# Kernel optimization log

Hardware: AMD Instinct MI355X
Metric: run time of the kernel (lower is better)

## Reference

```python
import jax, jax.numpy as jnp
import numpy as np

D_TEXT, D_AUDIO, D_HID = 1024, 768, 1024
EPS = 1e-5


def layer_norm(x, gamma, beta):
    mu = jnp.mean(x, axis=-1, keepdims=True)
    var = jnp.mean(jnp.square(x - mu), axis=-1, keepdims=True)
    return (x - mu) * jax.lax.rsqrt(var + EPS) * gamma + beta


def setup_inputs() -> dict:
    key = jax.random.key(0)
    ks = jax.random.split(key, 8)
    B, L, S = 16, 1024, 2048
    # xavier_uniform bound = sqrt(6/(fan_in+fan_out))
    def xavier(k, shape):
        bound = np.sqrt(6.0 / (shape[0] + shape[1]))
        return jax.random.uniform(k, shape, jnp.float32, -bound, bound)
    return {
        "H_l": jax.random.normal(ks[0], (B, L, D_TEXT), jnp.float32),
        "H_a": jax.random.normal(ks[1], (B, S, D_AUDIO), jnp.float32),
        "W_text": xavier(ks[2], (D_TEXT, D_HID)),
        "b_text": jnp.zeros((D_HID,), jnp.float32),
        "W_audio": xavier(ks[3], (D_AUDIO, D_HID)),
        "b_audio": jnp.zeros((D_HID,), jnp.float32),
        "W_out": xavier(ks[4], (D_HID, D_HID)),
        "b_out": jnp.zeros((D_HID,), jnp.float32),
        "g1": jnp.ones((D_HID,), jnp.float32),
        "beta1": jnp.zeros((D_HID,), jnp.float32),
        "g2": jnp.ones((D_HID,), jnp.float32),
        "beta2": jnp.zeros((D_HID,), jnp.float32),
        "g_out": jnp.ones((D_HID,), jnp.float32),
        "beta_out": jnp.zeros((D_HID,), jnp.float32),
    }


def reference(H_l, H_a, W_text, b_text, W_audio, b_audio, W_out, b_out,
              g1, beta1, g2, beta2, g_out, beta_out):
    # projections
    text_p = jnp.einsum('bld,dh->blh', H_l, W_text) + b_text    # [B,L,H]
    audio_p = jnp.einsum('bsd,dh->bsh', H_a, W_audio) + b_audio  # [B,S,H]
    Q = layer_norm(text_p, g1, beta1)
    K = layer_norm(audio_p, g2, beta2)
    V = audio_p
    scale = 1.0 / np.sqrt(D_HID).astype(np.float32)
    scores = jnp.einsum('blh,bsh->bls', Q, K) * scale            # [B,L,S]
    alpha = jax.nn.softmax(scores, axis=-1)
    # dropout is identity in eval mode
    H_hyper = jnp.einsum('bls,bsh->blh', alpha, V)               # [B,L,H]
    H_hyper = jnp.einsum('blh,hk->blk', H_hyper, W_out) + b_out
    return layer_norm(H_hyper + H_l, g_out, beta_out)
```

## Files before the change

kernel.cpp:

```cpp
#include <hip/hip_runtime.h>
#include <cstdio>

typedef unsigned short u16;
typedef __bf16 bf16x8 __attribute__((ext_vector_type(8)));
typedef float f32x4 __attribute__((ext_vector_type(4)));
typedef unsigned short us4 __attribute__((ext_vector_type(4)));
typedef unsigned short us8 __attribute__((ext_vector_type(8)));

__device__ __forceinline__ u16 f2bf(float f) {
    union { float f; unsigned u; } x; x.f = f;
    unsigned u = x.u + 0x7fffu + ((x.u >> 16) & 1u);
    return (u16)(u >> 16);
}
__device__ __forceinline__ float bf2f(u16 u) {
    union { unsigned u; float f; } x; x.u = ((unsigned)u) << 16;
    return x.f;
}


#define LDFRAG(base, row, koff) \
  (*(const bf16x8*)((const char*)(base) + (size_t)(row) * 128 + \
                    ((koff) ^ (((row) & 7) << 4))))

#define LOAD_A(QM) do { \
  _Pragma("unroll") for (int j = 0; j < 4; ++j) \
    _Pragma("unroll") for (int ks = 0; ks < 2; ++ks) \
      af[j][ks] = LDFRAG(pA, wr * 128 + (QM) * 64 + j * 16 + fr, ks * 64 + kg * 16); \
} while (0)

#define LOAD_B(QN) do { \
  _Pragma("unroll") for (int i = 0; i < 2; ++i) \
    _Pragma("unroll") for (int ks = 0; ks < 2; ++ks) \
      bfr[QN][i][ks] = LDFRAG(pB, wc * 64 + (QN) * 32 + i * 16 + fr, ks * 64 + kg * 16); \
} while (0)

#define MFMA_Q(QM, QN) do { \
  _Pragma("unroll") for (int j = 0; j < 4; ++j) \
    _Pragma("unroll") for (int i = 0; i < 2; ++i) \
      _Pragma("unroll") for (int ks = 0; ks < 2; ++ks) \
        acc[(QM) * 4 + j][(QN) * 2 + i] = __builtin_amdgcn_mfma_f32_16x16x32_bf16( \
            af[j][ks], bfr[QN][i][ks], acc[(QM) * 4 + j][(QN) * 2 + i], 0, 0, 0); \
} while (0)

#define PHASE_SYNC() do { \
  __builtin_amdgcn_s_barrier(); \
  asm volatile("s_waitcnt lgkmcnt(0)" ::: "memory"); \
  __builtin_amdgcn_sched_barrier(0); \
} while (0)

template<int TAG, bool HAS_BIAS, bool HAS_RESID, bool OUT_BF16>
__global__ __launch_bounds__(512, 2)
void gemm_nt(const u16* __restrict__ A, const u16* __restrict__ Bm,
             void* __restrict__ Cm, const float* __restrict__ bias,
             const float* __restrict__ resid,
             int K, int lda, int ldb, int ldc,
             long sA, long sB, long sC, float scale)
{
    __shared__ __align__(16) u16 lA[2 * 256 * 64];
    __shared__ __align__(16) u16 lB[2 * 256 * 64];

    const int tid = threadIdx.x;
    const long bz = blockIdx.z;
    A  += bz * sA;
    Bm += bz * sB;
    const long cbase = bz * sC;

    int bx, by;
    if (gridDim.z == 1) {
        const int gx = gridDim.x;
        const int flat = blockIdx.y * gx + blockIdx.x;
        const int q = (gx * gridDim.y) >> 3;
        const int wg = (flat & 7) * q + (flat >> 3);
        const int per = gx << 3;
        const int band = wg / per, rem = wg % per;
        bx = rem % gx;
        by = band * 8 + rem / gx;
    } else {
        bx = blockIdx.x; by = blockIdx.y;
    }
    const int m0 = by * 256;
    const int n0 = bx * 256;

    const int lane = tid & 63;
    const int w  = tid >> 6;
    const int wr = w >> 2, wc = w & 3;
    const int fr = lane & 15;
    const int kg = lane >> 4;

    auto stage_half = [&](int d_, int kt, int op, int h) {
        const u16* src = op ? Bm : A;
        const int  ld  = op ? ldb : lda;
        const int  bs  = op ? n0 : m0;
        u16* lds = (op ? lB : lA) + d_ * 16384 + h * 8192;
#pragma unroll
        for (int i2 = 0; i2 < 2; ++i2) {
            const int c  = i2 * 512 + tid;
            const int r  = c >> 3;
            const int kb = ((c & 7) * 16) ^ ((r & 7) << 4);
            const u16* g = src + (size_t)(bs + h * 128 + r) * ld + kt * 64 + (kb >> 1);
            __builtin_amdgcn_global_load_lds(
                (const __attribute__((address_space(1))) void*)g,
                (__attribute__((address_space(3))) void*)(lds + (size_t)c * 8), 16, 0, 0);
        }
    };
    auto stage_tile = [&](int d_, int kt) {
        stage_half(d_, kt, 0, 0); stage_half(d_, kt, 0, 1);
        stage_half(d_, kt, 1, 0); stage_half(d_, kt, 1, 1);
    };

    f32x4 acc[8][4] = {};
    bf16x8 af[4][2];
    bf16x8 bfr[2][2][2];

    const int nt = K >> 6;
    stage_tile(0, 0);

    for (int T = 0; T < nt; ++T) {
        const int d = T & 1;
        const u16* pA = lA + d * 16384;
        const u16* pB = lB + d * 16384;

        if (T + 1 < nt) {
            stage_tile(d ^ 1, T + 1);
            asm volatile("s_waitcnt vmcnt(8)" ::: "memory");
        } else {
            asm volatile("s_waitcnt vmcnt(0)" ::: "memory");
        }
        __builtin_amdgcn_s_barrier();

        LOAD_A(0); LOAD_B(0);
        PHASE_SYNC();
        __builtin_amdgcn_s_setprio(1); MFMA_Q(0, 0); __builtin_amdgcn_s_setprio(0);
        __builtin_amdgcn_s_barrier();

        LOAD_B(1);
        PHASE_SYNC();
        __builtin_amdgcn_s_setprio(1); MFMA_Q(0, 1); __builtin_amdgcn_s_setprio(0);
        __builtin_amdgcn_s_barrier();

        LOAD_A(1);
        PHASE_SYNC();
        __builtin_amdgcn_s_setprio(1); MFMA_Q(1, 0); __builtin_amdgcn_s_setprio(0);
        __builtin_amdgcn_s_barrier();

        __builtin_amdgcn_s_setprio(1); MFMA_Q(1, 1); __builtin_amdgcn_s_setprio(0);
    }

    const int orow = m0 + wr * 128 + kg * 4;
    const int ocol = n0 + wc * 64 + fr;
#pragma unroll
    for (int mf = 0; mf < 8; ++mf) {
#pragma unroll
        for (int r = 0; r < 4; ++r) {
            const int m = orow + mf * 16 + r;
#pragma unroll
            for (int nf = 0; nf < 4; ++nf) {
                const int n = ocol + nf * 16;
                float v = acc[mf][nf][r] * scale;
                if (HAS_BIAS)  v += bias[n];
                if (HAS_RESID) v += resid[cbase + (long)m * ldc + n];
                if (OUT_BF16)  ((u16*)Cm)[cbase + (long)m * ldc + n] = f2bf(v);
                else           ((float*)Cm)[cbase + (long)m * ldc + n] = v;
            }
        }
    }
}

template<bool IN_BF16, bool OUT_BF16>
__global__ __launch_bounds__(256)
void ln1024(const void* in, const float* __restrict__ g,
            const float* __restrict__ beta, void* out)
{
    const long row = blockIdx.x;
    const int tid = threadIdx.x;
    float x0, x1, x2, x3;
    if (IN_BF16) {
        const us4 v = ((const us4*)in)[row * 256 + tid];
        x0 = bf2f(v[0]); x1 = bf2f(v[1]); x2 = bf2f(v[2]); x3 = bf2f(v[3]);
    } else {
        const float4 v = ((const float4*)in)[row * 256 + tid];
        x0 = v.x; x1 = v.y; x2 = v.z; x3 = v.w;
    }
    float s  = x0 + x1 + x2 + x3;
    float s2 = x0 * x0 + x1 * x1 + x2 * x2 + x3 * x3;
#pragma unroll
    for (int off = 32; off > 0; off >>= 1) {
        s  += __shfl_xor(s, off);
        s2 += __shfl_xor(s2, off);
    }
    __shared__ float rs[4], rq[4];
    if ((tid & 63) == 0) { rs[tid >> 6] = s; rq[tid >> 6] = s2; }
    __syncthreads();
    const float S  = rs[0] + rs[1] + rs[2] + rs[3];
    const float S2 = rq[0] + rq[1] + rq[2] + rq[3];
    const float mu = S * (1.0f / 1024.0f);
    const float var = S2 * (1.0f / 1024.0f) - mu * mu;
    const float rstd = rsqrtf(var + 1e-5f);
    const float4 gg = ((const float4*)g)[tid];
    const float4 bb = ((const float4*)beta)[tid];
    const float y0 = (x0 - mu) * rstd * gg.x + bb.x;
    const float y1 = (x1 - mu) * rstd * gg.y + bb.y;
    const float y2 = (x2 - mu) * rstd * gg.z + bb.z;
    const float y3 = (x3 - mu) * rstd * gg.w + bb.w;
    if (OUT_BF16) {
        us4 o; o[0] = f2bf(y0); o[1] = f2bf(y1); o[2] = f2bf(y2); o[3] = f2bf(y3);
        ((us4*)out)[row * 256 + tid] = o;
    } else {
        float4 o; o.x = y0; o.y = y1; o.z = y2; o.w = y3;
        ((float4*)out)[row * 256 + tid] = o;
    }
}

__global__ __launch_bounds__(256)
void softmax2048_bf16(u16* io)
{
    const long row = blockIdx.x;
    const int tid = threadIdx.x;
    const us8 v = ((const us8*)io)[row * 256 + tid];
    float x[8];
#pragma unroll
    for (int i = 0; i < 8; ++i) x[i] = bf2f(v[i]);
    float m = x[0];
#pragma unroll
    for (int i = 1; i < 8; ++i) m = fmaxf(m, x[i]);
#pragma unroll
    for (int off = 32; off > 0; off >>= 1) m = fmaxf(m, __shfl_xor(m, off));
    __shared__ float rm[4], rsum[4];
    if ((tid & 63) == 0) rm[tid >> 6] = m;
    __syncthreads();
    m = fmaxf(fmaxf(rm[0], rm[1]), fmaxf(rm[2], rm[3]));
    float e[8];
    float s = 0.f;
#pragma unroll
    for (int i = 0; i < 8; ++i) { e[i] = __expf(x[i] - m); s += e[i]; }
#pragma unroll
    for (int off = 32; off > 0; off >>= 1) s += __shfl_xor(s, off);
    if ((tid & 63) == 0) rsum[tid >> 6] = s;
    __syncthreads();
    s = rsum[0] + rsum[1] + rsum[2] + rsum[3];
    const float inv = 1.0f / s;
    us8 o;
#pragma unroll
    for (int i = 0; i < 8; ++i) o[i] = f2bf(e[i] * inv);
    ((us8*)io)[row * 256 + tid] = o;
}

__global__ __launch_bounds__(256)
void cast_f32_bf16(const float* __restrict__ in, u16* __restrict__ out, long n8)
{
    const long i = (long)blockIdx.x * 256 + threadIdx.x;
    if (i >= n8) return;
    const float4 a = ((const float4*)in)[i * 2];
    const float4 b = ((const float4*)in)[i * 2 + 1];
    us8 o;
    o[0] = f2bf(a.x); o[1] = f2bf(a.y); o[2] = f2bf(a.z); o[3] = f2bf(a.w);
    o[4] = f2bf(b.x); o[5] = f2bf(b.y); o[6] = f2bf(b.z); o[7] = f2bf(b.w);
    ((us8*)out)[i] = o;
}

__global__ __launch_bounds__(256)
void tcast_f32_bf16(const float* __restrict__ in, u16* __restrict__ out,
                    int R, int C)
{
    __shared__ float t[32][33];
    const int tx = threadIdx.x, ty = threadIdx.y;
    const int c0 = blockIdx.x * 32, r0 = blockIdx.y * 32;
#pragma unroll
    for (int i = 0; i < 4; ++i)
        t[ty + i * 8][tx] = in[(long)(r0 + ty + i * 8) * C + c0 + tx];
    __syncthreads();
#pragma unroll
    for (int i = 0; i < 4; ++i)
        out[(long)(c0 + ty + i * 8) * R + r0 + tx] = f2bf(t[tx][ty + i * 8]);
}

__global__ __launch_bounds__(256)
void t_bf16_batched(const u16* __restrict__ in, u16* __restrict__ out,
                    int R, int C)
{
    __shared__ u16 t[32][34];
    const int tx = threadIdx.x, ty = threadIdx.y;
    const int c0 = blockIdx.x * 32, r0 = blockIdx.y * 32;
    const long base = (long)blockIdx.z * R * C;
#pragma unroll
    for (int i = 0; i < 4; ++i)
        t[ty + i * 8][tx] = in[base + (long)(r0 + ty + i * 8) * C + c0 + tx];
    __syncthreads();
#pragma unroll
    for (int i = 0; i < 4; ++i)
        out[base + (long)(c0 + ty + i * 8) * R + r0 + tx] = t[tx][ty + i * 8];
}

extern "C" void kernel_launch(void* const* d_in, const int* in_sizes, int n_in,
                              void* d_out, int out_size, void* d_ws, size_t ws_size,
                              hipStream_t stream)
{
    const float* H_l      = (const float*)d_in[0];
    const float* H_a      = (const float*)d_in[1];
    const float* W_text   = (const float*)d_in[2];
    const float* b_text   = (const float*)d_in[3];
    const float* W_audio  = (const float*)d_in[4];
    const float* b_audio  = (const float*)d_in[5];
    const float* W_out    = (const float*)d_in[6];
    const float* b_out    = (const float*)d_in[7];
    const float* g1       = (const float*)d_in[8];
    const float* beta1    = (const float*)d_in[9];
    const float* g2       = (const float*)d_in[10];
    const float* beta2    = (const float*)d_in[11];
    const float* g_out    = (const float*)d_in[12];
    const float* beta_out = (const float*)d_in[13];
    (void)in_sizes; (void)n_in; (void)out_size;

    const int B = 16, L = 1024, S = 2048, DT = 1024, DA = 768, H = 1024;

    char* ws = (char*)d_ws;
    const size_t SZ_HLB = (size_t)B * L * DT * 2;
    const size_t SZ_HAB = (size_t)B * S * DA * 2;
    const size_t O_A    = SZ_HLB + SZ_HAB;
    const size_t SZ_A   = (size_t)B * L * H * 2;
    const size_t O_C    = O_A + SZ_A;
    const size_t SZ_C   = (size_t)B * S * H * 2;
    const size_t O_D    = O_C + SZ_C;
    const size_t SZ_D   = (size_t)B * S * H * 2;
    const size_t O_W    = O_D + SZ_D;
    const size_t need   = O_W + (size_t)(DT * H + DA * H + H * H) * 2;

    if (ws_size < need) {
        fprintf(stderr, "[kernel_launch] ws_size=%zu < needed=%zu — aborting launches\n",
                ws_size, need);
        return;
    }

    u16*   Hlb     = (u16*)(ws);
    u16*   Hab     = (u16*)(ws + SZ_HLB);
    u16*   Scores  = (u16*)(ws);
    u16*   Abuf    = (u16*)(ws + O_A);
    u16*   Vbuf    = (u16*)(ws + O_C);
    u16*   Kbuf    = (u16*)(ws + O_D);
    float* OutPre  = (float*)(ws + O_D);
    u16*   Wt_text  = (u16*)(ws + O_W);
    u16*   Wt_audio = Wt_text + (size_t)DT * H;
    u16*   Wt_out   = Wt_audio + (size_t)DA * H;
    u16*   Vt      = (u16*)d_out;

    const float scale = 0.03125f;

    cast_f32_bf16<<<(B * L * DT / 8 + 255) / 256, 256, 0, stream>>>(H_l, Hlb, (long)B * L * DT / 8);
    cast_f32_bf16<<<(B * S * DA / 8 + 255) / 256, 256, 0, stream>>>(H_a, Hab, (long)B * S * DA / 8);
    tcast_f32_bf16<<<dim3(H / 32, DT / 32), dim3(32, 8), 0, stream>>>(W_text, Wt_text, DT, H);
    tcast_f32_bf16<<<dim3(H / 32, DA / 32), dim3(32, 8), 0, stream>>>(W_audio, Wt_audio, DA, H);
    tcast_f32_bf16<<<dim3(H / 32, H / 32),  dim3(32, 8), 0, stream>>>(W_out, Wt_out, H, H);

    gemm_nt<1, true, false, true><<<dim3(H / 256, B * L / 256, 1), 512, 0, stream>>>(
        Hlb, Wt_text, Abuf, b_text, nullptr, DT, DT, DT, H, 0, 0, 0, 1.0f);
    ln1024<true, true><<<B * L, 256, 0, stream>>>(Abuf, g1, beta1, Abuf);

    gemm_nt<2, true, false, true><<<dim3(H / 256, B * S / 256, 1), 512, 0, stream>>>(
        Hab, Wt_audio, Vbuf, b_audio, nullptr, DA, DA, DA, H, 0, 0, 0, 1.0f);
    ln1024<true, true><<<B * S, 256, 0, stream>>>(Vbuf, g2, beta2, Kbuf);

    t_bf16_batched<<<dim3(H / 32, S / 32, B), dim3(32, 8), 0, stream>>>(Vbuf, Vt, S, H);

    gemm_nt<3, false, false, true><<<dim3(S / 256, L / 256, B), 512, 0, stream>>>(
        Abuf, Kbuf, Scores, nullptr, nullptr, H, H, H, S,
        (long)L * H, (long)S * H, (long)L * S, scale);

    softmax2048_bf16<<<B * L, 256, 0, stream>>>(Scores);

    gemm_nt<5, false, false, true><<<dim3(H / 256, L / 256, B), 512, 0, stream>>>(
        Scores, Vt, Abuf, nullptr, nullptr, S, S, S, H,
        (long)L * S, (long)H * S, (long)L * H, 1.0f);

    gemm_nt<6, true, true, false><<<dim3(H / 256, B * L / 256, 1), 512, 0, stream>>>(
        Abuf, Wt_out, OutPre, b_out, H_l, H, H, H, H, 0, 0, 0, 1.0f);

    ln1024<false, false><<<B * L, 256, 0, stream>>>(OutPre, g_out, beta_out, (float*)d_out);
}
```

Measured before the change: 552.5 us.

## Fuse V transpose into audio GEMM epilogue, unify tile swizzle, relax barriers

The audio projection GEMM now writes a transposed bf16 copy of V directly from its epilogue, which removes the separate batched transpose kernel. The XCD-aware block swizzle now also applies to batched grids. The explicit lgkmcnt waits and sched_barriers after LDS fragment loads become plain barriers, leaving the compiler to insert the waits. The output projection stores its pre-LayerNorm result in bf16 rather than fp32, halving that traffic at some cost in precision. The transposed V stores are strided 8-byte writes, which may coalesce poorly.

```diff
diff --git a/kernel.cpp b/kernel.cpp
--- a/kernel.cpp
+++ b/kernel.cpp
@@ -42,17 +42,16 @@
             af[j][ks], bfr[QN][i][ks], acc[(QM) * 4 + j][(QN) * 2 + i], 0, 0, 0); \
 } while (0)
 
-#define PHASE_SYNC() do { \
+#define BARRIER() do { \
   __builtin_amdgcn_s_barrier(); \
-  asm volatile("s_waitcnt lgkmcnt(0)" ::: "memory"); \
-  __builtin_amdgcn_sched_barrier(0); \
+  asm volatile("" ::: "memory"); \
 } while (0)
 
-template<int TAG, bool HAS_BIAS, bool HAS_RESID, bool OUT_BF16>
+template<int TAG, bool HAS_BIAS, bool HAS_RESID, bool OUT_BF16, bool EMIT_VT>
 __global__ __launch_bounds__(512, 2)
 void gemm_nt(const u16* __restrict__ A, const u16* __restrict__ Bm,
              void* __restrict__ Cm, const float* __restrict__ bias,
-             const float* __restrict__ resid,
+             const float* __restrict__ resid, u16* __restrict__ vt,
              int K, int lda, int ldb, int ldc,
              long sA, long sB, long sC, float scale)
 {
@@ -60,24 +59,22 @@
     __shared__ __align__(16) u16 lB[2 * 256 * 64];
 
     const int tid = threadIdx.x;
-    const long bz = blockIdx.z;
+
+    const int gx = gridDim.x, gy = gridDim.y;
+    {
+    }
+    int flat = ((int)blockIdx.z * gy + blockIdx.y) * gx + blockIdx.x;
+    const int nwg = gx * gy * (int)gridDim.z;
+    const int q = nwg >> 3;
+    flat = (flat & 7) * q + (flat >> 3);
+    const int bx = flat % gx;
+    const int t2 = flat / gx;
+    const int by = t2 % gy;
+    const long bz = t2 / gy;
+
     A  += bz * sA;
     Bm += bz * sB;
     const long cbase = bz * sC;
-
-    int bx, by;
-    if (gridDim.z == 1) {
-        const int gx = gridDim.x;
-        const int flat = blockIdx.y * gx + blockIdx.x;
-        const int q = (gx * gridDim.y) >> 3;
-        const int wg = (flat & 7) * q + (flat >> 3);
-        const int per = gx << 3;
-        const int band = wg / per, rem = wg % per;
-        bx = rem % gx;
-        by = band * 8 + rem / gx;
-    } else {
-        bx = blockIdx.x; by = blockIdx.y;
-    }
     const int m0 = by * 256;
     const int n0 = bx * 256;
 
@@ -126,22 +123,22 @@
         } else {
             asm volatile("s_waitcnt vmcnt(0)" ::: "memory");
         }
-        __builtin_amdgcn_s_barrier();
+        BARRIER();
 
         LOAD_A(0); LOAD_B(0);
-        PHASE_SYNC();
+        BARRIER();
         __builtin_amdgcn_s_setprio(1); MFMA_Q(0, 0); __builtin_amdgcn_s_setprio(0);
-        __builtin_amdgcn_s_barrier();
+        BARRIER();
 
         LOAD_B(1);
-        PHASE_SYNC();
+        BARRIER();
         __builtin_amdgcn_s_setprio(1); MFMA_Q(0, 1); __builtin_amdgcn_s_setprio(0);
-        __builtin_amdgcn_s_barrier();
+        BARRIER();
 
         LOAD_A(1);
-        PHASE_SYNC();
+        BARRIER();
         __builtin_amdgcn_s_setprio(1); MFMA_Q(1, 0); __builtin_amdgcn_s_setprio(0);
-        __builtin_amdgcn_s_barrier();
+        BARRIER();
 
         __builtin_amdgcn_s_setprio(1); MFMA_Q(1, 1); __builtin_amdgcn_s_setprio(0);
     }
@@ -150,17 +147,28 @@
     const int ocol = n0 + wc * 64 + fr;
 #pragma unroll
     for (int mf = 0; mf < 8; ++mf) {
-#pragma unroll
-        for (int r = 0; r < 4; ++r) {
-            const int m = orow + mf * 16 + r;
-#pragma unroll
-            for (int nf = 0; nf < 4; ++nf) {
-                const int n = ocol + nf * 16;
+        const int mbase = orow + mf * 16;
+#pragma unroll
+        for (int nf = 0; nf < 4; ++nf) {
+            const int n = ocol + nf * 16;
+            float v4[4];
+#pragma unroll
+            for (int r = 0; r < 4; ++r) {
+                const int m = mbase + r;
                 float v = acc[mf][nf][r] * scale;
                 if (HAS_BIAS)  v += bias[n];
                 if (HAS_RESID) v += resid[cbase + (long)m * ldc + n];
+                v4[r] = v;
                 if (OUT_BF16)  ((u16*)Cm)[cbase + (long)m * ldc + n] = f2bf(v);
                 else           ((float*)Cm)[cbase + (long)m * ldc + n] = v;
+            }
+            if (EMIT_VT) {
+                const long b  = mbase >> 11;
+                const int  s  = mbase & 2047;
+                us4 o;
+#pragma unroll
+                for (int r = 0; r < 4; ++r) o[r] = f2bf(v4[r]);
+                *(us4*)(vt + (b * 1024 + n) * 2048 + s) = o;
             }
         }
     }
@@ -274,23 +282,6 @@
         out[(long)(c0 + ty + i * 8) * R + r0 + tx] = f2bf(t[tx][ty + i * 8]);
 }
 
-__global__ __launch_bounds__(256)
-void t_bf16_batched(const u16* __restrict__ in, u16* __restrict__ out,
-                    int R, int C)
-{
-    __shared__ u16 t[32][34];
-    const int tx = threadIdx.x, ty = threadIdx.y;
-    const int c0 = blockIdx.x * 32, r0 = blockIdx.y * 32;
-    const long base = (long)blockIdx.z * R * C;
-#pragma unroll
-    for (int i = 0; i < 4; ++i)
-        t[ty + i * 8][tx] = in[base + (long)(r0 + ty + i * 8) * C + c0 + tx];
-    __syncthreads();
-#pragma unroll
-    for (int i = 0; i < 4; ++i)
-        out[base + (long)(c0 + ty + i * 8) * R + r0 + tx] = t[tx][ty + i * 8];
-}
-
 extern "C" void kernel_launch(void* const* d_in, const int* in_sizes, int n_in,
                               void* d_out, int out_size, void* d_ws, size_t ws_size,
                               hipStream_t stream)
@@ -337,7 +328,7 @@
     u16*   Abuf    = (u16*)(ws + O_A);
     u16*   Vbuf    = (u16*)(ws + O_C);
     u16*   Kbuf    = (u16*)(ws + O_D);
-    float* OutPre  = (float*)(ws + O_D);
+    u16*   OutPre  = (u16*)(ws + O_D);
     u16*   Wt_text  = (u16*)(ws + O_W);
     u16*   Wt_audio = Wt_text + (size_t)DT * H;
     u16*   Wt_out   = Wt_audio + (size_t)DA * H;
@@ -351,28 +342,26 @@
     tcast_f32_bf16<<<dim3(H / 32, DA / 32), dim3(32, 8), 0, stream>>>(W_audio, Wt_audio, DA, H);
     tcast_f32_bf16<<<dim3(H / 32, H / 32),  dim3(32, 8), 0, stream>>>(W_out, Wt_out, H, H);
 
-    gemm_nt<1, true, false, true><<<dim3(H / 256, B * L / 256, 1), 512, 0, stream>>>(
-        Hlb, Wt_text, Abuf, b_text, nullptr, DT, DT, DT, H, 0, 0, 0, 1.0f);
+    gemm_nt<1, true, false, true, false><<<dim3(H / 256, B * L / 256, 1), 512, 0, stream>>>(
+        Hlb, Wt_text, Abuf, b_text, nullptr, nullptr, DT, DT, DT, H, 0, 0, 0, 1.0f);
     ln1024<true, true><<<B * L, 256, 0, stream>>>(Abuf, g1, beta1, Abuf);
 
-    gemm_nt<2, true, false, true><<<dim3(H / 256, B * S / 256, 1), 512, 0, stream>>>(
-        Hab, Wt_audio, Vbuf, b_audio, nullptr, DA, DA, DA, H, 0, 0, 0, 1.0f);
+    gemm_nt<2, true, false, true, true><<<dim3(H / 256, B * S / 256, 1), 512, 0, stream>>>(
+        Hab, Wt_audio, Vbuf, b_audio, nullptr, Vt, DA, DA, DA, H, 0, 0, 0, 1.0f);
     ln1024<true, true><<<B * S, 256, 0, stream>>>(Vbuf, g2, beta2, Kbuf);
 
-    t_bf16_batched<<<dim3(H / 32, S / 32, B), dim3(32, 8), 0, stream>>>(Vbuf, Vt, S, H);
-
-    gemm_nt<3, false, false, true><<<dim3(S / 256, L / 256, B), 512, 0, stream>>>(
-        Abuf, Kbuf, Scores, nullptr, nullptr, H, H, H, S,
+    gemm_nt<3, false, false, true, false><<<dim3(S / 256, L / 256, B), 512, 0, stream>>>(
+        Abuf, Kbuf, Scores, nullptr, nullptr, nullptr, H, H, H, S,
         (long)L * H, (long)S * H, (long)L * S, scale);
 
     softmax2048_bf16<<<B * L, 256, 0, stream>>>(Scores);
 
-    gemm_nt<5, false, false, true><<<dim3(H / 256, L / 256, B), 512, 0, stream>>>(
-        Scores, Vt, Abuf, nullptr, nullptr, S, S, S, H,
+    gemm_nt<5, false, false, true, false><<<dim3(H / 256, L / 256, B), 512, 0, stream>>>(
+        Scores, Vt, Abuf, nullptr, nullptr, nullptr, S, S, S, H,
         (long)L * S, (long)H * S, (long)L * H, 1.0f);
 
-    gemm_nt<6, true, true, false><<<dim3(H / 256, B * L / 256, 1), 512, 0, stream>>>(
-        Abuf, Wt_out, OutPre, b_out, H_l, H, H, H, H, 0, 0, 0, 1.0f);
-
-    ln1024<false, false><<<B * L, 256, 0, stream>>>(OutPre, g_out, beta_out, (float*)d_out);
-}
+    gemm_nt<6, true, true, true, false><<<dim3(H / 256, B * L / 256, 1), 512, 0, stream>>>(
+        Abuf, Wt_out, OutPre, b_out, H_l, nullptr, H, H, H, H, 0, 0, 0, 1.0f);
+
+    ln1024<true, false><<<B * L, 256, 0, stream>>>(OutPre, g_out, beta_out, (float*)d_out);
+}
```

Measured after the change: 535.6 us. 1.03x faster.
